# Kernel optimization log

Hardware: AMD Instinct MI355X
Metric: run time of the kernel (lower is better)

Reference implementation:

```python
import jax, jax.numpy as jnp
import numpy as np

B, N, E, H = 2, 20000, 400000, 128
COORDS_WEIGHT = 1.0


def setup_inputs() -> dict:
    key = jax.random.key(0)
    ks = jax.random.split(key, 12)

    def lin(k, i, o, scale=1.0):
        return (jax.random.normal(k, (i, o), jnp.float32) / np.sqrt(i)) * scale

    return {
        "h": jax.random.normal(ks[0], (B, N, H), jnp.float32),
        "coord": jax.random.normal(ks[1], (B, N, 3), jnp.float32),
        "others": jax.random.normal(ks[2], (B, N, H), jnp.float32),
        "edge_index": jax.random.randint(ks[3], (2, E), 0, N),
        "edge_w1": lin(ks[4], 2 * H + 1, H),
        "edge_b1": jnp.zeros((H,), jnp.float32),
        "edge_w2": lin(ks[5], H, H),
        "edge_b2": jnp.zeros((H,), jnp.float32),
        "node_w1": lin(ks[6], 3 * H, H),
        "node_b1": jnp.zeros((H,), jnp.float32),
        "node_w2": lin(ks[7], H, H),
        "node_b2": jnp.zeros((H,), jnp.float32),
        "coord_w1": lin(ks[8], H, H),
        "coord_b1": jnp.zeros((H,), jnp.float32),
        "coord_w2": lin(ks[9], H, 1, scale=0.001),  # xavier gain=0.001, no bias
    }


def reference(h, coord, others, edge_index, edge_w1, edge_b1, edge_w2, edge_b2,
              node_w1, node_b1, node_w2, node_b2, coord_w1, coord_b1, coord_w2):
    row, col = edge_index[0], edge_index[1]
    n_nodes = h.shape[1]

    # coord2radial_X: per-edge coordinate difference and squared distance
    coord_diff = coord[:, row] - coord[:, col]               # [B, E, 3]
    radial = jnp.sum(coord_diff ** 2, axis=-1, keepdims=True)  # [B, E, 1]

    # edge_model_X: gather endpoints, concat with radial, 2-layer ReLU MLP
    src, tgt = h[:, row], h[:, col]                          # [B, E, H]
    e = jnp.concatenate([src, tgt, radial], axis=-1)         # [B, E, 2H+1]
    e = jax.nn.relu(e @ edge_w1 + edge_b1)
    edge_feat = jax.nn.relu(e @ edge_w2 + edge_b2)           # [B, E, H]

    # coord_model_X: trans = coord_diff * coord_mlp(edge_feat); segment-mean over row
    gate = jax.nn.relu(edge_feat @ coord_w1 + coord_b1) @ coord_w2  # [B, E, 1]
    trans = coord_diff * gate                                # [B, E, 3]
    agg_t = jnp.zeros_like(coord).at[:, row].add(trans)      # [B, N, 3]
    cnt = jnp.zeros((n_nodes, 1), coord.dtype).at[row].add(1.0)
    cnt = jnp.maximum(cnt, 1.0)
    f = (agg_t / cnt) * COORDS_WEIGHT
    coord_out = coord + f                                    # [B, N, 3]

    # node_model_X: unsorted_segment_sum over row, concat [others, h, agg], MLP + residual
    agg = jnp.zeros_like(h).at[:, row].add(edge_feat)        # [B, N, H]
    a = jnp.concatenate([others, h, agg], axis=-1)           # [B, N, 3H]
    o = jax.nn.relu(a @ node_w1 + node_b1) @ node_w2 + node_b2
    h_out = h + o                                            # recurrent residual

    # pack node features and coordinates into one output array [B, N, H+3]
    return jnp.concatenate([h_out, coord_out], axis=-1)
```

## Files before the change

kernel.cpp:

```cpp
#include <hip/hip_runtime.h>
#include <cstddef>

#define BN 2
#define NN 20000
#define NE 400000
#define HH 128

typedef __attribute__((ext_vector_type(8))) short bf16x8;
typedef __attribute__((ext_vector_type(4))) float f32x4;
typedef unsigned short ushort_t;

__device__ __forceinline__ unsigned short f2b(float f) {
    unsigned u = __float_as_uint(f);
    unsigned r = (u + 0x7FFFu + ((u >> 16) & 1u)) >> 16;
    return (unsigned short)r;
}
__device__ __forceinline__ float b2f(ushort_t v) {
    return __uint_as_float(((unsigned)v) << 16);
}

__device__ __forceinline__ void gll16(const void* g, void* l) {
    __builtin_amdgcn_global_load_lds(
        (const __attribute__((address_space(1))) unsigned int*)g,
        (__attribute__((address_space(3))) unsigned int*)l,
        16, 0, 0);
}

__global__ void cvt_h_kernel(const float4* __restrict__ src, uint2* __restrict__ dst, int n4) {
    int i = blockIdx.x * 256 + threadIdx.x;
    if (i >= n4) return;
    float4 v = src[i];
    uint2 o;
    o.x = (unsigned)f2b(v.x) | ((unsigned)f2b(v.y) << 16);
    o.y = (unsigned)f2b(v.z) | ((unsigned)f2b(v.w) << 16);
    dst[i] = o;
}

__global__ void pack_w_kernel(const float* __restrict__ W, ushort_t* __restrict__ dst, int K) {
    int slot = blockIdx.x * 256 + threadIdx.x;
    int total = (K >> 6) * 1024;
    if (slot >= total) return;
    int l = slot & 63, nt = (slot >> 6) & 7, kt2 = (slot >> 9) & 1, c = slot >> 10;
    int col = nt * 16 + (l & 15);
    int k0 = c * 64 + kt2 * 32 + ((l >> 4) * 8);
    unsigned out[4];
    #pragma unroll
    for (int p = 0; p < 4; ++p) {
        unsigned lo = f2b(W[(size_t)(k0 + 2 * p) * HH + col]);
        unsigned hi = f2b(W[(size_t)(k0 + 2 * p + 1) * HH + col]);
        out[p] = lo | (hi << 16);
    }
    uint4* d = (uint4*)&dst[(size_t)slot * 8];
    *d = make_uint4(out[0], out[1], out[2], out[3]);
}

__global__ void hist_kernel(const int* __restrict__ eidx, int* __restrict__ histI) {
    int e = blockIdx.x * 256 + threadIdx.x;
    if (e >= NE) return;
    atomicAdd(&histI[eidx[e]], 1);
}

__global__ void scan_kernel(const int* __restrict__ histI, int* __restrict__ cursor,
                            float* __restrict__ cnt) {
    __shared__ int part[256];
    const int t = threadIdx.x;
    const int chunk = (NN + 255) / 256;
    const int lo = t * chunk, hi = min(lo + chunk, NN);
    int s = 0;
    for (int i = lo; i < hi; ++i) s += histI[i];
    part[t] = s;
    __syncthreads();
    for (int d = 1; d < 256; d <<= 1) {
        int v = (t >= d) ? part[t - d] : 0;
        __syncthreads();
        part[t] += v;
        __syncthreads();
    }
    int run = part[t] - s;
    for (int i = lo; i < hi; ++i) {
        cursor[i] = run;
        int hv = histI[i];
        cnt[i] = (float)hv;
        run += hv;
    }
}

__global__ void scatter_kernel(const int* __restrict__ eidx, int* __restrict__ cursor,
                               int* __restrict__ rowS, int* __restrict__ colS) {
    int e = blockIdx.x * 256 + threadIdx.x;
    if (e >= NE) return;
    const int r = eidx[e];
    int p = atomicAdd(&cursor[r], 1);
    rowS[p] = r;
    colS[p] = eidx[NE + e];
}

#define MFMA_FA(BB)                                                               \
    _Pragma("unroll")                                                             \
    for (int ktg = 0; ktg < 4; ++ktg) {                                           \
        _Pragma("unroll")                                                         \
        for (int mt = 0; mt < 8; ++mt) {                                          \
            bf16x8 a = *(const bf16x8*)&FA[((ktg * 8 + mt) * 64 + l) * 8];        \
            acc[mt][0] = __builtin_amdgcn_mfma_f32_16x16x32_bf16(                 \
                a, bw[(BB) + ktg * 2 + 0], acc[mt][0], 0, 0, 0);                  \
            acc[mt][1] = __builtin_amdgcn_mfma_f32_16x16x32_bf16(                 \
                a, bw[(BB) + ktg * 2 + 1], acc[mt][1], 0, 0, 0);                  \
        }                                                                         \
    }

#define MFMA_YN(BB)                                                               \
    _Pragma("unroll")                                                             \
    for (int ktg = 0; ktg < 4; ++ktg) {                                           \
        _Pragma("unroll")                                                         \
        for (int mt = 0; mt < 8; ++mt) {                                          \
            const int row_ = mt * 16 + lo16;                                      \
            bf16x8 a = *(const bf16x8*)&YN[row_ * 136 + ktg * 32 + hi4 * 8];      \
            acc[mt][0] = __builtin_amdgcn_mfma_f32_16x16x32_bf16(                 \
                a, bw[(BB) + ktg * 2 + 0], acc[mt][0], 0, 0, 0);                  \
            acc[mt][1] = __builtin_amdgcn_mfma_f32_16x16x32_bf16(                 \
                a, bw[(BB) + ktg * 2 + 1], acc[mt][1], 0, 0, 0);                  \
        }                                                                         \
    }

__global__ __launch_bounds__(256, 4)
void edge_kernel(const ushort_t* __restrict__ hbf, const float* __restrict__ coord,
                 const int* __restrict__ rowS, const int* __restrict__ colS,
                 const ushort_t* __restrict__ w1p, const ushort_t* __restrict__ w2p,
                 const ushort_t* __restrict__ cw1p,
                 const float* __restrict__ w1, const float* __restrict__ b1,
                 const float* __restrict__ b2, const float* __restrict__ cb1,
                 const float* __restrict__ cw2,
                 float* __restrict__ agg, float* __restrict__ aggt)
{
    __shared__ ushort_t SH[128 * 136];
    __shared__ int Rw[129], Cw[128];
    __shared__ float CD3[128 * 3];
    __shared__ float Rad[128];
    __shared__ float GT[128];

    ushort_t* const FA = SH;
    ushort_t* const YN = SH;

    const int t = threadIdx.x;
    const int l = t & 63;
    const int w = t >> 6;
    const int b = blockIdx.y;
    const int e0 = blockIdx.x * 128;

    const int lo16 = l & 15;
    const int hi4 = l >> 4;
    const int col0 = w * 32 + lo16;
    const int col1 = col0 + 16;

    bf16x8 bw[16];
    #pragma unroll
    for (int ktg = 0; ktg < 8; ++ktg) {
        bw[ktg * 2 + 0] = *(const bf16x8*)&w1p[((ktg * 8 + w * 2 + 0) * 64 + l) * 8];
        bw[ktg * 2 + 1] = *(const bf16x8*)&w1p[((ktg * 8 + w * 2 + 1) * 64 + l) * 8];
    }

    if (t < 128) {
        int r = rowS[e0 + t], c = colS[e0 + t];
        Rw[t] = r; Cw[t] = c; GT[t] = 0.0f;
        if (t == 0) Rw[128] = -1;
        const float* cr = coord + ((size_t)b * NN + r) * 3;
        const float* cc = coord + ((size_t)b * NN + c) * 3;
        float d0 = cr[0] - cc[0], d1 = cr[1] - cc[1], d2 = cr[2] - cc[2];
        CD3[t * 3] = d0; CD3[t * 3 + 1] = d1; CD3[t * 3 + 2] = d2;
        Rad[t] = d0 * d0 + d1 * d1 + d2 * d2;
    }

    f32x4 acc[8][2];
    #pragma unroll
    for (int mt = 0; mt < 8; ++mt) { acc[mt][0] = (f32x4)0.0f; acc[mt][1] = (f32x4)0.0f; }

    __syncthreads();

    #pragma unroll
    for (int i = 0; i < 2; ++i) {
        const int mt = w * 2 + i;
        const ushort_t* hb = hbf + ((size_t)b * NN + Rw[mt * 16 + lo16]) * HH + hi4 * 8;
        #pragma unroll
        for (int ktg = 0; ktg < 4; ++ktg)
            gll16(hb + ktg * 32, (void*)&FA[((ktg * 8 + mt) * 64) * 8]);
    }
    __syncthreads();

    MFMA_FA(0)
    __syncthreads();

    #pragma unroll
    for (int i = 0; i < 2; ++i) {
        const int mt = w * 2 + i;
        const ushort_t* hb = hbf + ((size_t)b * NN + Cw[mt * 16 + lo16]) * HH + hi4 * 8;
        #pragma unroll
        for (int ktg = 0; ktg < 4; ++ktg)
            gll16(hb + ktg * 32, (void*)&FA[((ktg * 8 + mt) * 64) * 8]);
    }
    __syncthreads();

    MFMA_FA(8)

    #pragma unroll
    for (int ktg = 0; ktg < 4; ++ktg) {
        bw[ktg * 2 + 0] = *(const bf16x8*)&w2p[((ktg * 8 + w * 2 + 0) * 64 + l) * 8];
        bw[ktg * 2 + 1] = *(const bf16x8*)&w2p[((ktg * 8 + w * 2 + 1) * 64 + l) * 8];
        bw[8 + ktg * 2 + 0] = *(const bf16x8*)&cw1p[((ktg * 8 + w * 2 + 0) * 64 + l) * 8];
        bw[8 + ktg * 2 + 1] = *(const bf16x8*)&cw1p[((ktg * 8 + w * 2 + 1) * 64 + l) * 8];
    }

    __syncthreads();

    {
        const float w1r0 = w1[256 * HH + col0];
        const float w1r1 = w1[256 * HH + col1];
        const float b10 = b1[col0], b11 = b1[col1];
        #pragma unroll
        for (int mt = 0; mt < 8; ++mt)
            #pragma unroll
            for (int j = 0; j < 4; ++j) {
                const int row = mt * 16 + hi4 * 4 + j;
                const float r = Rad[row];
                float v0 = fmaxf(acc[mt][0][j] + r * w1r0 + b10, 0.0f);
                float v1 = fmaxf(acc[mt][1][j] + r * w1r1 + b11, 0.0f);
                YN[row * 136 + col0] = f2b(v0);
                YN[row * 136 + col1] = f2b(v1);
                acc[mt][0][j] = 0.0f; acc[mt][1][j] = 0.0f;
            }
    }
    __syncthreads();

    MFMA_YN(0)
    __syncthreads();

    {
        const float b20 = b2[col0], b21 = b2[col1];
        #pragma unroll
        for (int mt = 0; mt < 8; ++mt)
            #pragma unroll
            for (int j = 0; j < 4; ++j) {
                const int row = mt * 16 + hi4 * 4 + j;
                float v0 = fmaxf(acc[mt][0][j] + b20, 0.0f);
                float v1 = fmaxf(acc[mt][1][j] + b21, 0.0f);
                YN[row * 136 + col0] = f2b(v0);
                YN[row * 136 + col1] = f2b(v1);
                acc[mt][0][j] = 0.0f; acc[mt][1][j] = 0.0f;
            }
    }
    __syncthreads();

    MFMA_YN(8)

    {
        const int colc = t & 127;
        const int half = t >> 7;
        const int r0 = half * 64;
        float s = 0.0f;
        for (int r = r0; r < r0 + 64; ++r) {
            s += b2f(YN[r * 136 + colc]);
            if (r == r0 + 63 || Rw[r] != Rw[r + 1]) {
                atomicAdd(&agg[((size_t)b * NN + Rw[r]) * HH + colc], s);
                s = 0.0f;
            }
        }
    }

    {
        const float cbA = cb1[col0], cbB = cb1[col1];
        const float cwA = cw2[col0], cwB = cw2[col1];
        #pragma unroll
        for (int mt = 0; mt < 8; ++mt)
            #pragma unroll
            for (int j = 0; j < 4; ++j) {
                float g = fmaxf(acc[mt][0][j] + cbA, 0.0f) * cwA
                        + fmaxf(acc[mt][1][j] + cbB, 0.0f) * cwB;
                g += __shfl_xor(g, 1);
                g += __shfl_xor(g, 2);
                g += __shfl_xor(g, 4);
                g += __shfl_xor(g, 8);
                if (lo16 == 0)
                    atomicAdd(&GT[mt * 16 + hi4 * 4 + j], g);
            }
    }
    __syncthreads();

    if (t < 128) {
        const bool head = (t == 0) || (Rw[t] != Rw[t - 1]);
        if (head) {
            float s0 = 0.0f, s1 = 0.0f, s2 = 0.0f;
            int r = t;
            const int myrow = Rw[t];
            while (r < 128 && Rw[r] == myrow) {
                const float g = GT[r];
                s0 += CD3[r * 3 + 0] * g;
                s1 += CD3[r * 3 + 1] * g;
                s2 += CD3[r * 3 + 2] * g;
                ++r;
            }
            const size_t base = ((size_t)b * NN + myrow) * 3;
            atomicAdd(&aggt[base + 0], s0);
            atomicAdd(&aggt[base + 1], s1);
            atomicAdd(&aggt[base + 2], s2);
        }
    }
}

__global__ __launch_bounds__(256, 2)
void node_kernel(const ushort_t* __restrict__ hbf, const float* __restrict__ h,
                 const float* __restrict__ coord, const float* __restrict__ others,
                 const float* __restrict__ agg,
                 const ushort_t* __restrict__ nw1p, const ushort_t* __restrict__ nw2p,
                 const float* __restrict__ nb1, const float* __restrict__ nb2,
                 const float* __restrict__ aggt, const float* __restrict__ cnt,
                 float* __restrict__ out)
{
    __shared__ ushort_t SH[128 * 136];
    ushort_t* const FA = SH;
    ushort_t* const YN = SH;

    const int t = threadIdx.x;
    const int l = t & 63;
    const int w = t >> 6;
    const int b = blockIdx.y;
    const int n0 = blockIdx.x * 128;

    const int lo16 = l & 15;
    const int hi4 = l >> 4;
    const int col0 = w * 32 + lo16;
    const int col1 = col0 + 16;

    bf16x8 bw[24];
    #pragma unroll
    for (int ktg = 0; ktg < 12; ++ktg) {
        bw[ktg * 2 + 0] = *(const bf16x8*)&nw1p[((ktg * 8 + w * 2 + 0) * 64 + l) * 8];
        bw[ktg * 2 + 1] = *(const bf16x8*)&nw1p[((ktg * 8 + w * 2 + 1) * 64 + l) * 8];
    }

    if (t < 128) {
        const int n = n0 + t;
        if (n < NN) {
            const float rinv = 1.0f / fmaxf(cnt[n], 1.0f);
            const float* cp = coord + ((size_t)b * NN + n) * 3;
            const float* ap = aggt + ((size_t)b * NN + n) * 3;
            float* op = out + ((size_t)b * NN + n) * 131 + HH;
            op[0] = cp[0] + ap[0] * rinv;
            op[1] = cp[1] + ap[1] * rinv;
            op[2] = cp[2] + ap[2] * rinv;
        }
    }

    f32x4 acc[8][2];
    #pragma unroll
    for (int mt = 0; mt < 8; ++mt) { acc[mt][0] = (f32x4)0.0f; acc[mt][1] = (f32x4)0.0f; }

    #define STAGE_CVT(SRC)                                                        \
        _Pragma("unroll")                                                         \
        for (int i = 0; i < 2; ++i) {                                             \
            const int mt = w * 2 + i;                                             \
            const int row = min(n0 + mt * 16 + lo16, NN - 1);                     \
            const float* p = (SRC) + ((size_t)b * NN + row) * HH + hi4 * 8;       \
            _Pragma("unroll")                                                     \
            for (int ktg = 0; ktg < 4; ++ktg) {                                   \
                float4 fa = *(const float4*)(p + ktg * 32);                       \
                float4 fb = *(const float4*)(p + ktg * 32 + 4);                   \
                uint4 u;                                                          \
                u.x = (unsigned)f2b(fa.x) | ((unsigned)f2b(fa.y) << 16);          \
                u.y = (unsigned)f2b(fa.z) | ((unsigned)f2b(fa.w) << 16);          \
                u.z = (unsigned)f2b(fb.x) | ((unsigned)f2b(fb.y) << 16);          \
                u.w = (unsigned)f2b(fb.z) | ((unsigned)f2b(fb.w) << 16);          \
                *(uint4*)&FA[((ktg * 8 + mt) * 64 + l) * 8] = u;                  \
            }                                                                     \
        }

    STAGE_CVT(others)
    __syncthreads();
    MFMA_FA(0)
    __syncthreads();

    #pragma unroll
    for (int i = 0; i < 2; ++i) {
        const int mt = w * 2 + i;
        const int row = min(n0 + mt * 16 + lo16, NN - 1);
        const ushort_t* hb = hbf + ((size_t)b * NN + row) * HH + hi4 * 8;
        #pragma unroll
        for (int ktg = 0; ktg < 4; ++ktg)
            gll16(hb + ktg * 32, (void*)&FA[((ktg * 8 + mt) * 64) * 8]);
    }
    __syncthreads();
    MFMA_FA(8)
    __syncthreads();

    STAGE_CVT(agg)
    __syncthreads();
    MFMA_FA(16)

    #pragma unroll
    for (int ktg = 0; ktg < 4; ++ktg) {
        bw[ktg * 2 + 0] = *(const bf16x8*)&nw2p[((ktg * 8 + w * 2 + 0) * 64 + l) * 8];
        bw[ktg * 2 + 1] = *(const bf16x8*)&nw2p[((ktg * 8 + w * 2 + 1) * 64 + l) * 8];
    }

    __syncthreads();

    {
        const float b10 = nb1[col0], b11 = nb1[col1];
        #pragma unroll
        for (int mt = 0; mt < 8; ++mt)
            #pragma unroll
            for (int j = 0; j < 4; ++j) {
                const int row = mt * 16 + hi4 * 4 + j;
                float v0 = fmaxf(acc[mt][0][j] + b10, 0.0f);
                float v1 = fmaxf(acc[mt][1][j] + b11, 0.0f);
                YN[row * 136 + col0] = f2b(v0);
                YN[row * 136 + col1] = f2b(v1);
                acc[mt][0][j] = 0.0f; acc[mt][1][j] = 0.0f;
            }
    }
    __syncthreads();

    MFMA_YN(0)

    {
        const float b20 = nb2[col0], b21 = nb2[col1];
        #pragma unroll
        for (int mt = 0; mt < 8; ++mt)
            #pragma unroll
            for (int j = 0; j < 4; ++j) {
                const int rowg = n0 + mt * 16 + hi4 * 4 + j;
                if (rowg < NN) {
                    const size_t rb = (size_t)b * NN + rowg;
                    out[rb * 131 + col0] = h[rb * HH + col0] + acc[mt][0][j] + b20;
                    out[rb * 131 + col1] = h[rb * HH + col1] + acc[mt][1][j] + b21;
                }
            }
    }
}

extern "C" void kernel_launch(void* const* d_in, const int* in_sizes, int n_in,
                              void* d_out, int out_size, void* d_ws, size_t ws_size,
                              hipStream_t stream)
{
    const float* h      = (const float*)d_in[0];
    const float* coord  = (const float*)d_in[1];
    const float* others = (const float*)d_in[2];
    const int*   eidx   = (const int*)d_in[3];
    const float* w1  = (const float*)d_in[4];
    const float* b1  = (const float*)d_in[5];
    const float* w2  = (const float*)d_in[6];
    const float* b2  = (const float*)d_in[7];
    const float* nw1 = (const float*)d_in[8];
    const float* nb1 = (const float*)d_in[9];
    const float* nw2 = (const float*)d_in[10];
    const float* nb2 = (const float*)d_in[11];
    const float* cw1 = (const float*)d_in[12];
    const float* cb1 = (const float*)d_in[13];
    const float* cw2 = (const float*)d_in[14];
    float* out = (float*)d_out;

    float* agg   = (float*)d_ws;
    float* aggt  = agg + (size_t)BN * NN * HH;
    int*   histI = (int*)(aggt + (size_t)BN * NN * 3);
    float* cnt   = (float*)(histI + NN);
    int*   cursor= (int*)(cnt + NN);
    int*   rowS  = cursor + NN;
    int*   colS  = rowS + NE;
    ushort_t* hbf  = (ushort_t*)(colS + NE);
    ushort_t* w1p  = hbf + (size_t)BN * NN * HH;
    ushort_t* w2p  = w1p + 32768;
    ushort_t* cw1p = w2p + 16384;
    ushort_t* nw1p = cw1p + 16384;
    ushort_t* nw2p = nw1p + 49152;

    const size_t zero_bytes =
        ((size_t)BN * NN * HH + (size_t)BN * NN * 3 + NN) * sizeof(float);
    hipMemsetAsync(d_ws, 0, zero_bytes, stream);

    const int n4 = (BN * NN * HH) / 4;
    cvt_h_kernel<<<n4 / 256, 256, 0, stream>>>((const float4*)h, (uint2*)hbf, n4);
    pack_w_kernel<<<16, 256, 0, stream>>>(w1, w1p, 256);
    pack_w_kernel<<<8, 256, 0, stream>>>(w2, w2p, 128);
    pack_w_kernel<<<8, 256, 0, stream>>>(cw1, cw1p, 128);
    pack_w_kernel<<<24, 256, 0, stream>>>(nw1, nw1p, 384);
    pack_w_kernel<<<8, 256, 0, stream>>>(nw2, nw2p, 128);

    hist_kernel<<<(NE + 255) / 256, 256, 0, stream>>>(eidx, histI);
    scan_kernel<<<1, 256, 0, stream>>>(histI, cursor, cnt);
    scatter_kernel<<<(NE + 255) / 256, 256, 0, stream>>>(eidx, cursor, rowS, colS);

    dim3 eg(NE / 128, BN);
    edge_kernel<<<eg, 256, 0, stream>>>(hbf, coord, rowS, colS, w1p, w2p, cw1p,
                                        w1, b1, b2, cb1, cw2, agg, aggt);

    dim3 ng((NN + 127) / 128, BN);
    node_kernel<<<ng, 256, 0, stream>>>(hbf, h, coord, others, agg,
                                        nw1p, nw2p, nb1, nb2, aggt, cnt, out);
}
```

Baseline: 489.5 us.

## Remap edge tiles per XCD and halve node kernel tile to 64 rows

The edge kernel remaps blockIdx.x so that each of the 8 XCDs processes a contiguous range of sorted edge tiles. This should improve L2 locality for gathers and atomics on nearby rows. The node kernel tile shrinks from 128 to 64 nodes per block, with new 4-row-tile MFMA macros and a smaller LDS buffer. That doubles the node-kernel grid for better CU occupancy and load balance, at the cost of reloading the weights more often.

```diff
diff --git a/kernel.cpp b/kernel.cpp
--- a/kernel.cpp
+++ b/kernel.cpp
@@ -145,7 +145,12 @@
     const int l = t & 63;
     const int w = t >> 6;
     const int b = blockIdx.y;
-    const int e0 = blockIdx.x * 128;
+
+    const int nwg = gridDim.x;
+    const int q = nwg >> 3, r8 = nwg & 7;
+    const int xcd = blockIdx.x & 7, pos = blockIdx.x >> 3;
+    const int tile = (xcd < r8 ? xcd * (q + 1) : r8 * (q + 1) + (xcd - r8) * q) + pos;
+    const int e0 = tile * 128;
 
     const int lo16 = l & 15;
     const int hi4 = l >> 4;
@@ -305,6 +310,33 @@
     }
 }
 
+#define MFMA_FA4(BB)                                                              \
+    _Pragma("unroll")                                                             \
+    for (int ktg = 0; ktg < 4; ++ktg) {                                           \
+        _Pragma("unroll")                                                         \
+        for (int mt = 0; mt < 4; ++mt) {                                          \
+            bf16x8 a = *(const bf16x8*)&FA[((ktg * 4 + mt) * 64 + l) * 8];        \
+            acc[mt][0] = __builtin_amdgcn_mfma_f32_16x16x32_bf16(                 \
+                a, bw[(BB) + ktg * 2 + 0], acc[mt][0], 0, 0, 0);                  \
+            acc[mt][1] = __builtin_amdgcn_mfma_f32_16x16x32_bf16(                 \
+                a, bw[(BB) + ktg * 2 + 1], acc[mt][1], 0, 0, 0);                  \
+        }                                                                         \
+    }
+
+#define MFMA_YN4(BB)                                                              \
+    _Pragma("unroll")                                                             \
+    for (int ktg = 0; ktg < 4; ++ktg) {                                           \
+        _Pragma("unroll")                                                         \
+        for (int mt = 0; mt < 4; ++mt) {                                          \
+            const int row_ = mt * 16 + lo16;                                      \
+            bf16x8 a = *(const bf16x8*)&YN[row_ * 136 + ktg * 32 + hi4 * 8];      \
+            acc[mt][0] = __builtin_amdgcn_mfma_f32_16x16x32_bf16(                 \
+                a, bw[(BB) + ktg * 2 + 0], acc[mt][0], 0, 0, 0);                  \
+            acc[mt][1] = __builtin_amdgcn_mfma_f32_16x16x32_bf16(                 \
+                a, bw[(BB) + ktg * 2 + 1], acc[mt][1], 0, 0, 0);                  \
+        }                                                                         \
+    }
+
 __global__ __launch_bounds__(256, 2)
 void node_kernel(const ushort_t* __restrict__ hbf, const float* __restrict__ h,
                  const float* __restrict__ coord, const float* __restrict__ others,
@@ -314,7 +346,7 @@
                  const float* __restrict__ aggt, const float* __restrict__ cnt,
                  float* __restrict__ out)
 {
-    __shared__ ushort_t SH[128 * 136];
+    __shared__ ushort_t SH[64 * 136];
     ushort_t* const FA = SH;
     ushort_t* const YN = SH;
 
@@ -322,7 +354,7 @@
     const int l = t & 63;
     const int w = t >> 6;
     const int b = blockIdx.y;
-    const int n0 = blockIdx.x * 128;
+    const int n0 = blockIdx.x * 64;
 
     const int lo16 = l & 15;
     const int hi4 = l >> 4;
@@ -336,7 +368,7 @@
         bw[ktg * 2 + 1] = *(const bf16x8*)&nw1p[((ktg * 8 + w * 2 + 1) * 64 + l) * 8];
     }
 
-    if (t < 128) {
+    if (t < 64) {
         const int n = n0 + t;
         if (n < NN) {
             const float rinv = 1.0f / fmaxf(cnt[n], 1.0f);
@@ -349,14 +381,13 @@
         }
     }
 
-    f32x4 acc[8][2];
-    #pragma unroll
-    for (int mt = 0; mt < 8; ++mt) { acc[mt][0] = (f32x4)0.0f; acc[mt][1] = (f32x4)0.0f; }
+    f32x4 acc[4][2];
+    #pragma unroll
+    for (int mt = 0; mt < 4; ++mt) { acc[mt][0] = (f32x4)0.0f; acc[mt][1] = (f32x4)0.0f; }
 
     #define STAGE_CVT(SRC)                                                        \
-        _Pragma("unroll")                                                         \
-        for (int i = 0; i < 2; ++i) {                                             \
-            const int mt = w * 2 + i;                                             \
+        {                                                                         \
+            const int mt = w;                                                     \
             const int row = min(n0 + mt * 16 + lo16, NN - 1);                     \
             const float* p = (SRC) + ((size_t)b * NN + row) * HH + hi4 * 8;       \
             _Pragma("unroll")                                                     \
@@ -368,31 +399,30 @@
                 u.y = (unsigned)f2b(fa.z) | ((unsigned)f2b(fa.w) << 16);          \
                 u.z = (unsigned)f2b(fb.x) | ((unsigned)f2b(fb.y) << 16);          \
                 u.w = (unsigned)f2b(fb.z) | ((unsigned)f2b(fb.w) << 16);          \
-                *(uint4*)&FA[((ktg * 8 + mt) * 64 + l) * 8] = u;                  \
+                *(uint4*)&FA[((ktg * 4 + mt) * 64 + l) * 8] = u;                  \
             }                                                                     \
         }
 
     STAGE_CVT(others)
     __syncthreads();
-    MFMA_FA(0)
-    __syncthreads();
-
-    #pragma unroll
-    for (int i = 0; i < 2; ++i) {
-        const int mt = w * 2 + i;
+    MFMA_FA4(0)
+    __syncthreads();
+
+    {
+        const int mt = w;
         const int row = min(n0 + mt * 16 + lo16, NN - 1);
         const ushort_t* hb = hbf + ((size_t)b * NN + row) * HH + hi4 * 8;
         #pragma unroll
         for (int ktg = 0; ktg < 4; ++ktg)
-            gll16(hb + ktg * 32, (void*)&FA[((ktg * 8 + mt) * 64) * 8]);
-    }
-    __syncthreads();
-    MFMA_FA(8)
+            gll16(hb + ktg * 32, (void*)&FA[((ktg * 4 + mt) * 64) * 8]);
+    }
+    __syncthreads();
+    MFMA_FA4(8)
     __syncthreads();
 
     STAGE_CVT(agg)
     __syncthreads();
-    MFMA_FA(16)
+    MFMA_FA4(16)
 
     #pragma unroll
     for (int ktg = 0; ktg < 4; ++ktg) {
@@ -405,7 +435,7 @@
     {
         const float b10 = nb1[col0], b11 = nb1[col1];
         #pragma unroll
-        for (int mt = 0; mt < 8; ++mt)
+        for (int mt = 0; mt < 4; ++mt)
             #pragma unroll
             for (int j = 0; j < 4; ++j) {
                 const int row = mt * 16 + hi4 * 4 + j;
@@ -418,12 +448,12 @@
     }
     __syncthreads();
 
-    MFMA_YN(0)
+    MFMA_YN4(0)
 
     {
         const float b20 = nb2[col0], b21 = nb2[col1];
         #pragma unroll
-        for (int mt = 0; mt < 8; ++mt)
+        for (int mt = 0; mt < 4; ++mt)
             #pragma unroll
             for (int j = 0; j < 4; ++j) {
                 const int rowg = n0 + mt * 16 + hi4 * 4 + j;
@@ -491,7 +521,7 @@
     edge_kernel<<<eg, 256, 0, stream>>>(hbf, coord, rowS, colS, w1p, w2p, cw1p,
                                         w1, b1, b2, cb1, cw2, agg, aggt);
 
-    dim3 ng((NN + 127) / 128, BN);
+    dim3 ng((NN + 63) / 64, BN);
     node_kernel<<<ng, 256, 0, stream>>>(hbf, h, coord, others, agg,
                                         nw1p, nw2p, nb1, nb2, aggt, cnt, out);
 }
```

New measurement: 489.9 us. No clear change (+0.1%).
